# Optimization experiments

Hardware: AMD Instinct MI355X
Metric: run time of the kernel (lower is better)

## Reference

```python
import jax, jax.numpy as jnp
import numpy as np

N, E, IN_C, HID_C, OUT_C = 50000, 800000, 64, 64, 8
NEG_SLOPE = 0.2


def setup_inputs() -> dict:
    key = jax.random.key(0)
    ks = jax.random.split(key, 12)
    return {
        "x": jax.random.normal(ks[0], (N, IN_C), dtype=jnp.float32),
        "edge_index": jax.random.randint(ks[1], (2, E), 0, N, dtype=jnp.int64),
        "edge_value": jax.random.uniform(ks[2], (E,), dtype=jnp.float32),
        "W1": jax.random.normal(ks[3], (IN_C, HID_C), dtype=jnp.float32) * 0.1,
        "a1_src": jax.random.normal(ks[4], (HID_C,), dtype=jnp.float32) * 0.1,
        "a1_dst": jax.random.normal(ks[5], (HID_C,), dtype=jnp.float32) * 0.1,
        "b1": jnp.zeros((HID_C,), dtype=jnp.float32),
        "W2": jax.random.normal(ks[6], (HID_C, OUT_C), dtype=jnp.float32) * 0.1,
        "a2_src": jax.random.normal(ks[7], (OUT_C,), dtype=jnp.float32) * 0.1,
        "a2_dst": jax.random.normal(ks[8], (OUT_C,), dtype=jnp.float32) * 0.1,
        "b2": jnp.zeros((OUT_C,), dtype=jnp.float32),
    }


def _rgat_conv(x, src, dst, edge_value, W, a_src, a_dst, b, n_nodes):
    # Linear transform: [N, out_c]
    h = x @ W
    # Per-node attention halves, gathered per edge -> per-edge logit
    e_src = h @ a_src  # [N]
    e_dst = h @ a_dst  # [N]
    logits = jax.nn.leaky_relu(e_src[src] + e_dst[dst], negative_slope=NEG_SLOPE)  # [E]
    # Segment softmax over destination neighborhoods (numerically stable)
    m = jax.ops.segment_max(logits, dst, num_segments=n_nodes)  # [N]
    ex = jnp.exp(logits - m[dst])
    denom = jax.ops.segment_sum(ex, dst, num_segments=n_nodes)  # [N]
    alpha = ex / (denom[dst] + 1e-16)  # [E]
    # Edge-weighted messages, scatter-aggregate to destinations
    msg = (alpha * edge_value)[:, None] * h[src]  # [E, out_c]
    out = jax.ops.segment_sum(msg, dst, num_segments=n_nodes)  # [N, out_c]
    return out + b


def reference(x, edge_index, edge_value, W1, a1_src, a1_dst, b1, W2, a2_src, a2_dst, b2):
    src, dst = edge_index[0], edge_index[1]
    n = x.shape[0]
    hid = _rgat_conv(x, src, dst, edge_value, W1, a1_src, a1_dst, b1, n)
    hid = jax.nn.relu(hid)
    out = _rgat_conv(hid, src, dst, edge_value, W2, a2_src, a2_dst, b2, n)
    return jax.nn.log_softmax(out, axis=1)
```

## Files before the change

### kernel.cpp

```cpp
#include <hip/hip_runtime.h>
#include <hip/hip_fp16.h>
#include <math.h>


#define CHUNK 4096
#define NBKT  256
#define CAP   6144

typedef unsigned long long ull;
typedef float v2f __attribute__((ext_vector_type(2)));

struct PartSmem {
    int lhist[NBKT], lbase[NBKT], lcur[NBKT], gbase[NBKT];
    ull buf[CHUNK];
};
struct GemmSmem {
    float4 Wl[64 * 16];
    float  Xt[64 * 64];
};
union FusedSmem { PartSmem p; GemmSmem g; };


__global__ void __launch_bounds__(256) part_gemm_kernel(
    const int* __restrict__ src, const int* __restrict__ dst,
    const float* __restrict__ ev, int* __restrict__ bcnt,
    ull* __restrict__ ped, int E, int nchunks,
    const float* __restrict__ x, const float* __restrict__ W,
    const float* __restrict__ a_src, const float* __restrict__ a_dst,
    unsigned* __restrict__ h, float* __restrict__ es, float* __restrict__ ed,
    int N)
{
    __shared__ FusedSmem sm;
    const int t = threadIdx.x;

    if (blockIdx.x < nchunks) {
        int e0 = blockIdx.x * CHUNK;
        int cnt = min(CHUNK, E - e0);
        sm.p.lhist[t] = 0;
        __syncthreads();
        for (int i = t; i < cnt; i += 256)
            atomicAdd(&sm.p.lhist[dst[e0 + i] >> 8], 1);
        __syncthreads();
        int myc = sm.p.lhist[t];
        sm.p.lbase[t] = myc;
        __syncthreads();
        for (int o = 1; o < 256; o <<= 1) {
            int add = (t >= o) ? sm.p.lbase[t - o] : 0;
            __syncthreads();
            sm.p.lbase[t] += add;
            __syncthreads();
        }
        int excl = sm.p.lbase[t] - myc;
        sm.p.gbase[t] = myc ? atomicAdd(&bcnt[t], myc) : 0;
        __syncthreads();
        sm.p.lbase[t] = excl;
        sm.p.lcur[t] = excl;
        __syncthreads();
        for (int i = t; i < cnt; i += 256) {
            int e = e0 + i;
            int d = dst[e];
            int b = d >> 8;
            unsigned p = (unsigned)src[e] | ((unsigned)(d & 255) << 16)
                       | ((unsigned)b << 24);
            ull q = (ull)p | ((ull)__float_as_uint(ev[e]) << 32);
            int r = atomicAdd(&sm.p.lcur[b], 1);
            sm.p.buf[r] = q;
        }
        __syncthreads();
        for (int i = t; i < cnt; i += 256) {
            ull q = sm.p.buf[i];
            int b = (int)((q >> 24) & 255);
            ped[(size_t)b * CAP + sm.p.gbase[b] + i - sm.p.lbase[b]] = q;
        }
        return;
    }

    const int n0 = (blockIdx.x - nchunks) * 64;

    #pragma unroll
    for (int i = 0; i < 4; ++i)
        sm.g.Wl[t + i * 256] = ((const float4*)W)[t + i * 256];

    #pragma unroll
    for (int i = 0; i < 4; ++i) {
        int f   = t + i * 256;
        int row = f >> 4, kq = f & 15;
        int grow = n0 + row;
        float4 v = make_float4(0.f, 0.f, 0.f, 0.f);
        if (grow < N) v = ((const float4*)x)[(size_t)grow * 16 + kq];
        int rs = row ^ ((kq & 3) << 2);
        sm.g.Xt[(kq * 4 + 0) * 64 + rs] = v.x;
        sm.g.Xt[(kq * 4 + 1) * 64 + rs] = v.y;
        sm.g.Xt[(kq * 4 + 2) * 64 + rs] = v.z;
        sm.g.Xt[(kq * 4 + 3) * 64 + rs] = v.w;
    }

    const int tx = t & 15;
    const int ty = t >> 4;
    const float4 asv = ((const float4*)a_src)[tx];
    const float4 adv = ((const float4*)a_dst)[tx];
    __syncthreads();

    float4 acc0 = make_float4(0.f,0.f,0.f,0.f);
    float4 acc1 = make_float4(0.f,0.f,0.f,0.f);
    float4 acc2 = make_float4(0.f,0.f,0.f,0.f);
    float4 acc3 = make_float4(0.f,0.f,0.f,0.f);

    #pragma unroll 8
    for (int k = 0; k < 64; ++k) {
        int swz = (k >> 2) & 3;
        const float4 xr = *(const float4*)&sm.g.Xt[k * 64 + ((ty ^ swz) << 2)];
        const float4 wv = sm.g.Wl[k * 16 + tx];
        acc0.x += xr.x * wv.x; acc0.y += xr.x * wv.y;
        acc0.z += xr.x * wv.z; acc0.w += xr.x * wv.w;
        acc1.x += xr.y * wv.x; acc1.y += xr.y * wv.y;
        acc1.z += xr.y * wv.z; acc1.w += xr.y * wv.w;
        acc2.x += xr.z * wv.x; acc2.y += xr.z * wv.y;
        acc2.z += xr.z * wv.z; acc2.w += xr.z * wv.w;
        acc3.x += xr.w * wv.x; acc3.y += xr.w * wv.y;
        acc3.z += xr.w * wv.z; acc3.w += xr.w * wv.w;
    }

    float4 accs[4] = {acc0, acc1, acc2, acc3};
    #pragma unroll
    for (int r = 0; r < 4; ++r) {
        int grow = n0 + ty * 4 + r;
        float4 a = accs[r];
        if (grow < N) {
            int lo = __builtin_amdgcn_cvt_pk_fp8_f32(a.x, a.y, 0, false);
            int pk = __builtin_amdgcn_cvt_pk_fp8_f32(a.z, a.w, lo, true);
            h[(size_t)grow * 16 + tx] = (unsigned)pk;
        }
        float ps = a.x * asv.x + a.y * asv.y + a.z * asv.z + a.w * asv.w;
        float pd = a.x * adv.x + a.y * adv.y + a.z * adv.z + a.w * adv.w;
        #pragma unroll
        for (int o = 8; o > 0; o >>= 1) {
            ps += __shfl_xor(ps, o);
            pd += __shfl_xor(pd, o);
        }
        if (tx == 0 && grow < N) { es[grow] = ps; ed[grow] = pd; }
    }
}


__global__ void __launch_bounds__(1024) csr2_kernel(
    const ull* __restrict__ ped, const int* __restrict__ bcnt,
    int* __restrict__ off, int* __restrict__ deg,
    ull* __restrict__ csre, int N)
{
    __shared__ int cl[256], sc[256], cur[256];
    int b = blockIdx.x, t = threadIdx.x;
    const int cnt = min(bcnt[b], CAP);
    const size_t base = (size_t)b * CAP;
    if (t < 256) cl[t] = 0;
    __syncthreads();
    for (int i = t; i < cnt; i += 1024)
        atomicAdd(&cl[(int)((ped[base + i] >> 16) & 255)], 1);
    __syncthreads();
    int myc = (t < 256) ? cl[t] : 0;
    if (t < 256) sc[t] = myc;
    __syncthreads();
    for (int o = 1; o < 256; o <<= 1) {
        int add = (t >= o && t < 256) ? sc[t - o] : 0;
        __syncthreads();
        if (t < 256) sc[t] += add;
        __syncthreads();
    }
    if (t < 256) {
        int excl = sc[t] - myc;
        int node = b * 256 + t;
        if (node < N) { off[node] = (int)base + excl; deg[node] = myc; }
        cur[t] = excl;
    }
    __syncthreads();
    for (int i = t; i < cnt; i += 1024) {
        ull q = ped[base + i];
        int dloc = (int)((q >> 16) & 255);
        int pos = (int)base + atomicAdd(&cur[dloc], 1);
        csre[pos] = (q & 0xFFFFFFFF00000000ull) | (q & 0xFFFFull);
    }
}


__global__ void __launch_bounds__(256) agg64_fused_kernel(
    const int* __restrict__ off, const int* __restrict__ deg,
    const ull* __restrict__ csre,
    const float* __restrict__ es, const float* __restrict__ ed,
    const unsigned* __restrict__ h, const float* __restrict__ b1,
    const float* __restrict__ W2, const float* __restrict__ a2s,
    const float* __restrict__ a2d, float* __restrict__ h2,
    float* __restrict__ es2, float* __restrict__ ed2, int N)
{
    __shared__ float W2s[64 * 8];
    const int t = threadIdx.x;
    if (t < 128) ((float4*)W2s)[t] = ((const float4*)W2)[t];

    const int wid = t >> 6, lane = t & 63;
    const int grp = lane >> 3;
    const int sl  = lane & 7;
    const int gbase = grp << 3;
    const int n = (blockIdx.x * 4 + wid) * 8 + grp;
    __syncthreads();
    if (n >= N) return;

    const int   beg = off[n];
    const int   dg  = deg[n];
    const float edn = ed[n];

    const float4 b1a = *(const float4*)&b1[sl * 8];
    const float4 b1b = *(const float4*)&b1[sl * 8 + 4];

    float acc[8];
    #pragma unroll
    for (int k = 0; k < 8; ++k) acc[k] = 0.f;
    float den = 0.f;

    for (int j0 = 0; j0 < dg; j0 += 8) {
        const int jj  = j0 + sl;
        const int idx = beg + min(jj, dg - 1);
        const ull rec = csre[idx];
        const int sv  = (int)(rec & 0xFFFFull);
        const float evv = __uint_as_float((unsigned)(rec >> 32));
        float z = es[sv] + edn;
        float l = z > 0.f ? z : 0.2f * z;
        float q = (jj < dg) ? __expf(l) : 0.f;
        den += q;
        const float w = q * evv;
        #pragma unroll
        for (int ts = 0; ts < 8; ++ts) {
            const int   svt = __shfl(sv, gbase + ts);
            const float wt  = __shfl(w,  gbase + ts);
            const uint2 u = *(const uint2*)&h[(size_t)svt * 16 + sl * 2];
            v2f fa = __builtin_amdgcn_cvt_pk_f32_fp8((int)u.x, false);
            v2f fb = __builtin_amdgcn_cvt_pk_f32_fp8((int)u.x, true);
            v2f fc = __builtin_amdgcn_cvt_pk_f32_fp8((int)u.y, false);
            v2f fd = __builtin_amdgcn_cvt_pk_f32_fp8((int)u.y, true);
            acc[0] += wt * fa.x; acc[1] += wt * fa.y;
            acc[2] += wt * fb.x; acc[3] += wt * fb.y;
            acc[4] += wt * fc.x; acc[5] += wt * fc.y;
            acc[6] += wt * fd.x; acc[7] += wt * fd.y;
        }
    }

    den += __shfl_xor(den, 1);
    den += __shfl_xor(den, 2);
    den += __shfl_xor(den, 4);
    const float inv = 1.f / (den + 1e-16f);

    float hid[8];
    hid[0] = fmaxf(acc[0] * inv + b1a.x, 0.f);
    hid[1] = fmaxf(acc[1] * inv + b1a.y, 0.f);
    hid[2] = fmaxf(acc[2] * inv + b1a.z, 0.f);
    hid[3] = fmaxf(acc[3] * inv + b1a.w, 0.f);
    hid[4] = fmaxf(acc[4] * inv + b1b.x, 0.f);
    hid[5] = fmaxf(acc[5] * inv + b1b.y, 0.f);
    hid[6] = fmaxf(acc[6] * inv + b1b.z, 0.f);
    hid[7] = fmaxf(acc[7] * inv + b1b.w, 0.f);

    float p[8];
    #pragma unroll
    for (int o = 0; o < 8; ++o) p[o] = 0.f;
    #pragma unroll
    for (int k = 0; k < 8; ++k) {
        const float4 wA = *(const float4*)&W2s[(sl * 8 + k) * 8];
        const float4 wB = *(const float4*)&W2s[(sl * 8 + k) * 8 + 4];
        p[0] += hid[k] * wA.x; p[1] += hid[k] * wA.y;
        p[2] += hid[k] * wA.z; p[3] += hid[k] * wA.w;
        p[4] += hid[k] * wB.x; p[5] += hid[k] * wB.y;
        p[6] += hid[k] * wB.z; p[7] += hid[k] * wB.w;
    }
    float s4[4];
    {
        const bool hi = (sl & 1);
        #pragma unroll
        for (int k = 0; k < 4; ++k) {
            float keep = hi ? p[k + 4] : p[k];
            float send = hi ? p[k]     : p[k + 4];
            s4[k] = keep + __shfl_xor(send, 1);
        }
    }
    float s2[2];
    {
        const bool hi = (sl & 2);
        #pragma unroll
        for (int k = 0; k < 2; ++k) {
            float keep = hi ? s4[k + 2] : s4[k];
            float send = hi ? s4[k]     : s4[k + 2];
            s2[k] = keep + __shfl_xor(send, 2);
        }
    }
    float s1;
    {
        const bool hi = (sl & 4);
        float keep = hi ? s2[1] : s2[0];
        float send = hi ? s2[0] : s2[1];
        s1 = keep + __shfl_xor(send, 4);
    }
    const int olane = 4 * (sl & 1) + 2 * ((sl >> 1) & 1) + ((sl >> 2) & 1);

    float ts = s1 * a2s[olane];
    float td = s1 * a2d[olane];
    ts += __shfl_xor(ts, 1); td += __shfl_xor(td, 1);
    ts += __shfl_xor(ts, 2); td += __shfl_xor(td, 2);
    ts += __shfl_xor(ts, 4); td += __shfl_xor(td, 4);

    h2[(size_t)n * 8 + olane] = s1;
    if (sl == 0) { es2[n] = ts; ed2[n] = td; }
}


__global__ void __launch_bounds__(256) agg8_lsm_kernel(
    const int* __restrict__ off, const int* __restrict__ deg,
    const ull* __restrict__ csre,
    const float* __restrict__ es, const float* __restrict__ ed,
    const float* __restrict__ h2, const float* __restrict__ b,
    float* __restrict__ out, int N)
{
    const int t = threadIdx.x;
    const int wid = t >> 6, lane = t & 63;
    const int grp = lane >> 2;
    const int sl  = lane & 3;
    const int gbase = grp << 2;
    const int n = (blockIdx.x * 4 + wid) * 16 + grp;
    if (n >= N) return;

    const int   beg = off[n];
    const int   dg  = deg[n];
    const float edn = ed[n];
    const float bc0 = b[2 * sl], bc1 = b[2 * sl + 1];

    float a0 = 0.f, a1 = 0.f, den = 0.f;

    for (int j0 = 0; j0 < dg; j0 += 4) {
        const int jj  = j0 + sl;
        const int idx = beg + min(jj, dg - 1);
        const ull rec = csre[idx];
        const int sv  = (int)(rec & 0xFFFFull);
        const float evv = __uint_as_float((unsigned)(rec >> 32));
        float z = es[sv] + edn;
        float l = z > 0.f ? z : 0.2f * z;
        float q = (jj < dg) ? __expf(l) : 0.f;
        den += q;
        const float w = q * evv;
        #pragma unroll
        for (int ts = 0; ts < 4; ++ts) {
            const int   svt = __shfl(sv, gbase + ts);
            const float wt  = __shfl(w,  gbase + ts);
            const float2 f = *(const float2*)&h2[(size_t)svt * 8 + 2 * sl];
            a0 += wt * f.x;
            a1 += wt * f.y;
        }
    }

    den += __shfl_xor(den, 1);
    den += __shfl_xor(den, 2);
    const float inv = 1.f / (den + 1e-16f);
    float v0 = a0 * inv + bc0;
    float v1 = a1 * inv + bc1;

    float vm = fmaxf(v0, v1);
    vm = fmaxf(vm, __shfl_xor(vm, 1));
    vm = fmaxf(vm, __shfl_xor(vm, 2));
    float s = __expf(v0 - vm) + __expf(v1 - vm);
    s += __shfl_xor(s, 1);
    s += __shfl_xor(s, 2);
    float lse = vm + logf(s);
    *(float2*)&out[(size_t)n * 8 + 2 * sl] = make_float2(v0 - lse, v1 - lse);
}


extern "C" void kernel_launch(void* const* d_in, const int* in_sizes, int n_in,
                              void* d_out, int out_size, void* d_ws, size_t ws_size,
                              hipStream_t stream)
{
    const float* x   = (const float*)d_in[0];
    const int*   ei  = (const int*)d_in[1];
    const float* ev  = (const float*)d_in[2];
    const float* W1  = (const float*)d_in[3];
    const float* a1s = (const float*)d_in[4];
    const float* a1d = (const float*)d_in[5];
    const float* b1  = (const float*)d_in[6];
    const float* W2  = (const float*)d_in[7];
    const float* a2s = (const float*)d_in[8];
    const float* a2d = (const float*)d_in[9];
    const float* b2  = (const float*)d_in[10];
    float* out = (float*)d_out;

    const int N = in_sizes[0] / 64;
    const int E = in_sizes[2];
    const int* srcp = ei;
    const int* dstp = ei + E;
    const int nchunks = (E + CHUNK - 1) / CHUNK;
    const int ngemm   = (N + 63) / 64;
    const int nbuck = (N + 255) / 256;

    ull*   ped  = (ull*)d_ws;
    ull*   csre = ped + (size_t)NBKT * CAP;
    int*   bcnt = (int*)(csre + (size_t)NBKT * CAP);
    int*   off  = bcnt + NBKT;
    int*   deg  = off + N;
    float* es1  = (float*)(deg + N);
    float* ed1  = es1 + N;
    float* es2  = ed1 + N;
    float* ed2  = es2 + N;
    unsigned* h1 = (unsigned*)(ed2 + N);
    float* h2   = (float*)(h1 + (size_t)N * 16);

    hipMemsetAsync(bcnt, 0, NBKT * sizeof(int), stream);

    part_gemm_kernel<<<nchunks + ngemm, 256, 0, stream>>>(
        srcp, dstp, ev, bcnt, ped, E, nchunks,
        x, W1, a1s, a1d, h1, es1, ed1, N);

    csr2_kernel<<<nbuck, 1024, 0, stream>>>(ped, bcnt, off, deg, csre, N);

    agg64_fused_kernel<<<(N + 31) / 32, 256, 0, stream>>>(
        off, deg, csre, es1, ed1, h1, b1, W2, a2s, a2d, h2, es2, ed2, N);

    agg8_lsm_kernel<<<(N + 63) / 64, 256, 0, stream>>>(
        off, deg, csre, es2, ed2, h2, b2, out, N);
}
```

Baseline: 144.1 us.

## Replace bucket partition and CSR build with direct per-node slot scatter

The two-stage adjacency build is replaced by a single pass. Before, edges were bucketed by destination block and a separate kernel then sorted each bucket into CSR. Now each edge does one global atomicAdd on a per-destination counter and is written into a fixed-capacity slot array of 96 entries per node. This removes the csr2 kernel launch and its extra read/write pass over the edge records. In exchange it uses many scattered 8-byte writes and global atomics into a large padded buffer, and any node with more than 96 incoming edges silently loses the extra edges.

```diff
diff --git a/kernel.cpp b/kernel.cpp
--- a/kernel.cpp
+++ b/kernel.cpp
@@ -3,83 +3,48 @@
 #include <math.h>
 
 
-#define CHUNK 4096
-#define NBKT  256
-#define CAP   6144
+#define SCHUNK 4096
+#define CAPN   96
 
 typedef unsigned long long ull;
 typedef float v2f __attribute__((ext_vector_type(2)));
 
-struct PartSmem {
-    int lhist[NBKT], lbase[NBKT], lcur[NBKT], gbase[NBKT];
-    ull buf[CHUNK];
-};
 struct GemmSmem {
     float4 Wl[64 * 16];
     float  Xt[64 * 64];
 };
-union FusedSmem { PartSmem p; GemmSmem g; };
-
-
-__global__ void __launch_bounds__(256) part_gemm_kernel(
+
+
+__global__ void __launch_bounds__(256) scat_gemm_kernel(
     const int* __restrict__ src, const int* __restrict__ dst,
-    const float* __restrict__ ev, int* __restrict__ bcnt,
-    ull* __restrict__ ped, int E, int nchunks,
+    const float* __restrict__ ev, int* __restrict__ cnt,
+    ull* __restrict__ slots, int E, int nscat,
     const float* __restrict__ x, const float* __restrict__ W,
     const float* __restrict__ a_src, const float* __restrict__ a_dst,
     unsigned* __restrict__ h, float* __restrict__ es, float* __restrict__ ed,
     int N)
 {
-    __shared__ FusedSmem sm;
+    __shared__ GemmSmem sm;
     const int t = threadIdx.x;
 
-    if (blockIdx.x < nchunks) {
-        int e0 = blockIdx.x * CHUNK;
-        int cnt = min(CHUNK, E - e0);
-        sm.p.lhist[t] = 0;
-        __syncthreads();
-        for (int i = t; i < cnt; i += 256)
-            atomicAdd(&sm.p.lhist[dst[e0 + i] >> 8], 1);
-        __syncthreads();
-        int myc = sm.p.lhist[t];
-        sm.p.lbase[t] = myc;
-        __syncthreads();
-        for (int o = 1; o < 256; o <<= 1) {
-            int add = (t >= o) ? sm.p.lbase[t - o] : 0;
-            __syncthreads();
-            sm.p.lbase[t] += add;
-            __syncthreads();
-        }
-        int excl = sm.p.lbase[t] - myc;
-        sm.p.gbase[t] = myc ? atomicAdd(&bcnt[t], myc) : 0;
-        __syncthreads();
-        sm.p.lbase[t] = excl;
-        sm.p.lcur[t] = excl;
-        __syncthreads();
-        for (int i = t; i < cnt; i += 256) {
-            int e = e0 + i;
-            int d = dst[e];
-            int b = d >> 8;
-            unsigned p = (unsigned)src[e] | ((unsigned)(d & 255) << 16)
-                       | ((unsigned)b << 24);
-            ull q = (ull)p | ((ull)__float_as_uint(ev[e]) << 32);
-            int r = atomicAdd(&sm.p.lcur[b], 1);
-            sm.p.buf[r] = q;
-        }
-        __syncthreads();
-        for (int i = t; i < cnt; i += 256) {
-            ull q = sm.p.buf[i];
-            int b = (int)((q >> 24) & 255);
-            ped[(size_t)b * CAP + sm.p.gbase[b] + i - sm.p.lbase[b]] = q;
+    if (blockIdx.x < nscat) {
+        const int e0 = blockIdx.x * SCHUNK;
+        const int e1 = min(e0 + SCHUNK, E);
+        for (int e = e0 + t; e < e1; e += 256) {
+            const int d = dst[e];
+            const ull q = (ull)(unsigned)src[e]
+                        | ((ull)__float_as_uint(ev[e]) << 32);
+            const int pos = atomicAdd(&cnt[d], 1);
+            if (pos < CAPN) slots[(size_t)d * CAPN + pos] = q;
         }
         return;
     }
 
-    const int n0 = (blockIdx.x - nchunks) * 64;
+    const int n0 = (blockIdx.x - nscat) * 64;
 
     #pragma unroll
     for (int i = 0; i < 4; ++i)
-        sm.g.Wl[t + i * 256] = ((const float4*)W)[t + i * 256];
+        sm.Wl[t + i * 256] = ((const float4*)W)[t + i * 256];
 
     #pragma unroll
     for (int i = 0; i < 4; ++i) {
@@ -89,10 +54,10 @@
         float4 v = make_float4(0.f, 0.f, 0.f, 0.f);
         if (grow < N) v = ((const float4*)x)[(size_t)grow * 16 + kq];
         int rs = row ^ ((kq & 3) << 2);
-        sm.g.Xt[(kq * 4 + 0) * 64 + rs] = v.x;
-        sm.g.Xt[(kq * 4 + 1) * 64 + rs] = v.y;
-        sm.g.Xt[(kq * 4 + 2) * 64 + rs] = v.z;
-        sm.g.Xt[(kq * 4 + 3) * 64 + rs] = v.w;
+        sm.Xt[(kq * 4 + 0) * 64 + rs] = v.x;
+        sm.Xt[(kq * 4 + 1) * 64 + rs] = v.y;
+        sm.Xt[(kq * 4 + 2) * 64 + rs] = v.z;
+        sm.Xt[(kq * 4 + 3) * 64 + rs] = v.w;
     }
 
     const int tx = t & 15;
@@ -109,8 +74,8 @@
     #pragma unroll 8
     for (int k = 0; k < 64; ++k) {
         int swz = (k >> 2) & 3;
-        const float4 xr = *(const float4*)&sm.g.Xt[k * 64 + ((ty ^ swz) << 2)];
-        const float4 wv = sm.g.Wl[k * 16 + tx];
+        const float4 xr = *(const float4*)&sm.Xt[k * 64 + ((ty ^ swz) << 2)];
+        const float4 wv = sm.Wl[k * 16 + tx];
         acc0.x += xr.x * wv.x; acc0.y += xr.x * wv.y;
         acc0.z += xr.x * wv.z; acc0.w += xr.x * wv.w;
         acc1.x += xr.y * wv.x; acc1.y += xr.y * wv.y;
@@ -143,48 +108,8 @@
 }
 
 
-__global__ void __launch_bounds__(1024) csr2_kernel(
-    const ull* __restrict__ ped, const int* __restrict__ bcnt,
-    int* __restrict__ off, int* __restrict__ deg,
-    ull* __restrict__ csre, int N)
-{
-    __shared__ int cl[256], sc[256], cur[256];
-    int b = blockIdx.x, t = threadIdx.x;
-    const int cnt = min(bcnt[b], CAP);
-    const size_t base = (size_t)b * CAP;
-    if (t < 256) cl[t] = 0;
-    __syncthreads();
-    for (int i = t; i < cnt; i += 1024)
-        atomicAdd(&cl[(int)((ped[base + i] >> 16) & 255)], 1);
-    __syncthreads();
-    int myc = (t < 256) ? cl[t] : 0;
-    if (t < 256) sc[t] = myc;
-    __syncthreads();
-    for (int o = 1; o < 256; o <<= 1) {
-        int add = (t >= o && t < 256) ? sc[t - o] : 0;
-        __syncthreads();
-        if (t < 256) sc[t] += add;
-        __syncthreads();
-    }
-    if (t < 256) {
-        int excl = sc[t] - myc;
-        int node = b * 256 + t;
-        if (node < N) { off[node] = (int)base + excl; deg[node] = myc; }
-        cur[t] = excl;
-    }
-    __syncthreads();
-    for (int i = t; i < cnt; i += 1024) {
-        ull q = ped[base + i];
-        int dloc = (int)((q >> 16) & 255);
-        int pos = (int)base + atomicAdd(&cur[dloc], 1);
-        csre[pos] = (q & 0xFFFFFFFF00000000ull) | (q & 0xFFFFull);
-    }
-}
-
-
 __global__ void __launch_bounds__(256) agg64_fused_kernel(
-    const int* __restrict__ off, const int* __restrict__ deg,
-    const ull* __restrict__ csre,
+    const int* __restrict__ cnt, const ull* __restrict__ slots,
     const float* __restrict__ es, const float* __restrict__ ed,
     const unsigned* __restrict__ h, const float* __restrict__ b1,
     const float* __restrict__ W2, const float* __restrict__ a2s,
@@ -203,9 +128,9 @@
     __syncthreads();
     if (n >= N) return;
 
-    const int   beg = off[n];
-    const int   dg  = deg[n];
-    const float edn = ed[n];
+    const size_t beg = (size_t)n * CAPN;
+    const int    dg  = min(cnt[n], CAPN);
+    const float  edn = ed[n];
 
     const float4 b1a = *(const float4*)&b1[sl * 8];
     const float4 b1b = *(const float4*)&b1[sl * 8 + 4];
@@ -217,8 +142,7 @@
 
     for (int j0 = 0; j0 < dg; j0 += 8) {
         const int jj  = j0 + sl;
-        const int idx = beg + min(jj, dg - 1);
-        const ull rec = csre[idx];
+        const ull rec = slots[beg + min(jj, max(dg, 1) - 1)];
         const int sv  = (int)(rec & 0xFFFFull);
         const float evv = __uint_as_float((unsigned)(rec >> 32));
         float z = es[sv] + edn;
@@ -310,8 +234,7 @@
 
 
 __global__ void __launch_bounds__(256) agg8_lsm_kernel(
-    const int* __restrict__ off, const int* __restrict__ deg,
-    const ull* __restrict__ csre,
+    const int* __restrict__ cnt, const ull* __restrict__ slots,
     const float* __restrict__ es, const float* __restrict__ ed,
     const float* __restrict__ h2, const float* __restrict__ b,
     float* __restrict__ out, int N)
@@ -324,17 +247,16 @@
     const int n = (blockIdx.x * 4 + wid) * 16 + grp;
     if (n >= N) return;
 
-    const int   beg = off[n];
-    const int   dg  = deg[n];
-    const float edn = ed[n];
+    const size_t beg = (size_t)n * CAPN;
+    const int    dg  = min(cnt[n], CAPN);
+    const float  edn = ed[n];
     const float bc0 = b[2 * sl], bc1 = b[2 * sl + 1];
 
     float a0 = 0.f, a1 = 0.f, den = 0.f;
 
     for (int j0 = 0; j0 < dg; j0 += 4) {
         const int jj  = j0 + sl;
-        const int idx = beg + min(jj, dg - 1);
-        const ull rec = csre[idx];
+        const ull rec = slots[beg + min(jj, max(dg, 1) - 1)];
         const int sv  = (int)(rec & 0xFFFFull);
         const float evv = __uint_as_float((unsigned)(rec >> 32));
         float z = es[sv] + edn;
@@ -390,33 +312,27 @@
     const int E = in_sizes[2];
     const int* srcp = ei;
     const int* dstp = ei + E;
-    const int nchunks = (E + CHUNK - 1) / CHUNK;
-    const int ngemm   = (N + 63) / 64;
-    const int nbuck = (N + 255) / 256;
-
-    ull*   ped  = (ull*)d_ws;
-    ull*   csre = ped + (size_t)NBKT * CAP;
-    int*   bcnt = (int*)(csre + (size_t)NBKT * CAP);
-    int*   off  = bcnt + NBKT;
-    int*   deg  = off + N;
-    float* es1  = (float*)(deg + N);
-    float* ed1  = es1 + N;
-    float* es2  = ed1 + N;
-    float* ed2  = es2 + N;
+    const int nscat = (E + SCHUNK - 1) / SCHUNK;
+    const int ngemm = (N + 63) / 64;
+
+    ull*   slots = (ull*)d_ws;
+    int*   cnt   = (int*)(slots + (size_t)N * CAPN);
+    float* es1   = (float*)(cnt + N);
+    float* ed1   = es1 + N;
+    float* es2   = ed1 + N;
+    float* ed2   = es2 + N;
     unsigned* h1 = (unsigned*)(ed2 + N);
-    float* h2   = (float*)(h1 + (size_t)N * 16);
-
-    hipMemsetAsync(bcnt, 0, NBKT * sizeof(int), stream);
-
-    part_gemm_kernel<<<nchunks + ngemm, 256, 0, stream>>>(
-        srcp, dstp, ev, bcnt, ped, E, nchunks,
+    float* h2    = (float*)(h1 + (size_t)N * 16);
+
+    hipMemsetAsync(cnt, 0, (size_t)N * sizeof(int), stream);
+
+    scat_gemm_kernel<<<nscat + ngemm, 256, 0, stream>>>(
+        srcp, dstp, ev, cnt, slots, E, nscat,
         x, W1, a1s, a1d, h1, es1, ed1, N);
 
-    csr2_kernel<<<nbuck, 1024, 0, stream>>>(ped, bcnt, off, deg, csre, N);
-
     agg64_fused_kernel<<<(N + 31) / 32, 256, 0, stream>>>(
-        off, deg, csre, es1, ed1, h1, b1, W2, a2s, a2d, h2, es2, ed2, N);
+        cnt, slots, es1, ed1, h1, b1, W2, a2s, a2d, h2, es2, ed2, N);
 
     agg8_lsm_kernel<<<(N + 63) / 64, 256, 0, stream>>>(
-        off, deg, csre, es2, ed2, h2, b2, out, N);
+        cnt, slots, es2, ed2, h2, b2, out, N);
 }
```

Measured after the change: 158.2 us. 1.1x slower.
